# Kernel optimization log

Measured on AMD Instinct MI355X. Metric: run time of the kernel, lower is better.

The kernel has to match this reference:

```python
import jax, jax.numpy as jnp
import numpy as np

TOP_K = 2

def setup_inputs() -> dict:
    key = jax.random.key(0)
    k1, k2, k3, k4, k5 = jax.random.split(key, 5)
    B, S, D, E, H = 1, 2048, 2048, 8, 5632
    scale = 0.02
    return {
        "x": jax.random.normal(k1, (B, S, D), dtype=jnp.float32),
        "gate_w": jax.random.normal(k2, (E, D), dtype=jnp.float32) * scale,
        "w1": jax.random.normal(k3, (E, H, D), dtype=jnp.float32) * scale,
        "w2": jax.random.normal(k4, (E, D, H), dtype=jnp.float32) * scale,
        "w3": jax.random.normal(k5, (E, H, D), dtype=jnp.float32) * scale,
    }


def reference(x, gate_w, w1, w2, w3):
    # x: [B, S, D]; gate_w: [E, D]; w1/w3: [E, H, D]; w2: [E, D, H]
    B, S, D = x.shape
    E = gate_w.shape[0]
    xf = x.reshape(-1, D)                      # [T, D]
    T = xf.shape[0]

    # Gate (gate_softmax=False): topk on raw scores, softmax over the top-k
    scores = xf @ gate_w.T                     # [T, E]
    expert_weights, expert_indices = jax.lax.top_k(scores, TOP_K)
    expert_weights = jax.nn.softmax(expert_weights, axis=-1)  # [T, K]

    # Scatter top-k weights to a dense [T, E] combine matrix (zeros elsewhere)
    combine = jnp.zeros((T, E), dtype=xf.dtype).at[
        jnp.arange(T)[:, None], expert_indices
    ].add(expert_weights)

    # SwiGLU FFN per expert, batched over the (small, fixed) expert axis.
    # Math identical to masked dispatch since combine is zero off the top-k.
    h = jax.nn.silu(jnp.einsum("td,ehd->eth", xf, w1)) \
        * jnp.einsum("td,ehd->eth", xf, w3)    # [E, T, H]
    ye = jnp.einsum("eth,edh->etd", h, w2)     # [E, T, D]

    # Weighted combine of top-k expert outputs per token
    y = jnp.einsum("etd,te->td", ye, combine)  # [T, D]
    return y.reshape(B, S, D)
```

## Files before the change

kernel.cpp:

```cpp
#include <hip/hip_runtime.h>
#include <hip/hip_bf16.h>

#define T_TOK 2048
#define DIM   2048
#define NE    8
#define NH    5632

typedef __attribute__((ext_vector_type(4))) float f32x4;
typedef __attribute__((ext_vector_type(8))) short short8;
typedef __attribute__((ext_vector_type(4))) unsigned int u32x4;
typedef __attribute__((ext_vector_type(4))) float float4v;

__device__ inline unsigned short f2bf(float f) {
    unsigned u = __builtin_bit_cast(unsigned, f);
    u += 0x7fffu + ((u >> 16) & 1u);
    return (unsigned short)(u >> 16);
}

__device__ __forceinline__ short8 pack8(float4v a, float4v b) {
    short8 o;
    o[0]=(short)f2bf(a[0]); o[1]=(short)f2bf(a[1]); o[2]=(short)f2bf(a[2]); o[3]=(short)f2bf(a[3]);
    o[4]=(short)f2bf(b[0]); o[5]=(short)f2bf(b[1]); o[6]=(short)f2bf(b[2]); o[7]=(short)f2bf(b[3]);
    return o;
}

__device__ __forceinline__ short8 cvt8(f32x4 lo, f32x4 hi) {
    u32x4 L = __builtin_bit_cast(u32x4, lo);
    u32x4 H = __builtin_bit_cast(u32x4, hi);
    u32x4 r;
    r[0] = __builtin_amdgcn_perm(L[1], L[0], 0x07060302u);
    r[1] = __builtin_amdgcn_perm(L[3], L[2], 0x07060302u);
    r[2] = __builtin_amdgcn_perm(H[1], H[0], 0x07060302u);
    r[3] = __builtin_amdgcn_perm(H[3], H[2], 0x07060302u);
    return __builtin_bit_cast(short8, r);
}

__device__ __forceinline__ void glds16(const void* g, void* l) {
    __builtin_amdgcn_global_load_lds((const __attribute__((address_space(1))) void*)g,
                                     (__attribute__((address_space(3))) void*)l, 16, 0, 0);
}

__global__ void k_cvt(const float* __restrict__ src, unsigned short* __restrict__ dst, int n8) {
    int i = blockIdx.x * blockDim.x + threadIdx.x;
    if (i >= n8) return;
    const float4v* xv = (const float4v*)src;
    ((short8*)dst)[i] = pack8(xv[2 * i], xv[2 * i + 1]);
}

__global__ void k_gate(const float* __restrict__ x, const float* __restrict__ gw,
                       int* __restrict__ rt_e, float* __restrict__ rt_w, int* __restrict__ cnt) {
    int wid = threadIdx.x >> 6, lane = threadIdx.x & 63;
    int t = blockIdx.x * 4 + wid;
    if (t >= T_TOK) return;
    float acc[NE];
#pragma unroll
    for (int e = 0; e < NE; e++) acc[e] = 0.f;
    const float* xr = x + (size_t)t * DIM;
    for (int d = lane; d < DIM; d += 64) {
        float xv = xr[d];
#pragma unroll
        for (int e = 0; e < NE; e++) acc[e] += xv * gw[e * DIM + d];
    }
#pragma unroll
    for (int e = 0; e < NE; e++) {
        float v = acc[e];
#pragma unroll
        for (int off = 32; off; off >>= 1) v += __shfl_xor(v, off);
        acc[e] = v;
    }
    if (lane == 0) {
        int i0 = 0; float s0 = acc[0];
#pragma unroll
        for (int e = 1; e < NE; e++) if (acc[e] > s0) { s0 = acc[e]; i0 = e; }
        int i1 = -1; float s1 = -1e30f;
#pragma unroll
        for (int e = 0; e < NE; e++) if (e != i0 && acc[e] > s1) { s1 = acc[e]; i1 = e; }
        float w0 = 1.f / (1.f + expf(s1 - s0));
        rt_e[2 * t] = i0; rt_e[2 * t + 1] = i1;
        rt_w[2 * t] = w0; rt_w[2 * t + 1] = 1.f - w0;
        atomicAdd(&cnt[i0], 1);
        atomicAdd(&cnt[i1], 1);
    }
}

__global__ void k_base(const int* __restrict__ cnt, int* __restrict__ base, int* __restrict__ pb) {
    if (threadIdx.x == 0) {
        int s = 0, p = 0;
        for (int e = 0; e < NE; e++) {
            base[e] = s; pb[e] = p;
            s += cnt[e];
            p += ((cnt[e] + 127) >> 7) << 7;
        }
    }
}

__global__ void k_assign(const int* __restrict__ rt_e, const float* __restrict__ rt_w,
                         const int* __restrict__ base, int* __restrict__ run,
                         int* __restrict__ tok, float* __restrict__ tw) {
    int t = blockIdx.x * blockDim.x + threadIdx.x;
    if (t >= T_TOK) return;
#pragma unroll
    for (int k = 0; k < 2; k++) {
        int e = rt_e[2 * t + k];
        int p = atomicAdd(&run[e], 1);
        int g = base[e] + p;
        tok[g] = t;
        tw[g] = rt_w[2 * t + k];
    }
}

__global__ void k_xpack(const float* __restrict__ x,
                        const int* __restrict__ cnt, const int* __restrict__ base,
                        const int* __restrict__ pb, const int* __restrict__ tok,
                        unsigned short* __restrict__ xp) {
    int e = blockIdx.z, mt = blockIdx.y, kt = blockIdx.x;
    int c = cnt[e], m0 = mt * 128;
    if (m0 >= c) return;
    int gb = base[e];
    int ptile = (pb[e] >> 7) + mt;
    int lane = threadIdx.x & 63, w = threadIdx.x >> 6;
    int kc = lane & 7;
    unsigned short* db = xp + (size_t)ptile * 262144 + (size_t)kt * 8192;
#pragma unroll
    for (int it = 0; it < 4; ++it) {
        int rloc = it * 32 + w * 8 + (lane >> 3);
        int slot = m0 + rloc;
        int t = tok[gb + (slot < c ? slot : 0)];
        const float* s = x + (size_t)t * DIM + kt * 64 + kc * 8;
        *(short8*)(db + kc * 1024 + rloc * 8) = pack8(*(const float4v*)s, *(const float4v*)(s + 4));
    }
}

__launch_bounds__(256, 3)
__global__ void k_ffn1(const unsigned short* __restrict__ xp,
                       const float* __restrict__ w1, const float* __restrict__ w3,
                       const int* __restrict__ cnt, const int* __restrict__ pb,
                       unsigned short* __restrict__ hb, int nwg) {
    int bid = blockIdx.x;
    int swz = (bid & 7) * (nwg >> 3) + (bid >> 3);
    int mt = swz & 15;
    int r2 = swz >> 4;
    int nt = r2 % 88;
    int e  = r2 / 88;
    int c  = cnt[e];
    int m0 = mt * 128;
    if (m0 >= c) return;
    int ptile = (pb[e] >> 7) + mt;

    __shared__ unsigned short As[8192];
    __shared__ float B1f[4096];
    __shared__ float B3f[4096];

    int tid = threadIdx.x;
    int lane = tid & 63, w = tid >> 6;
    int wm = w >> 1, wn = w & 1;
    int half = w & 1, wh = w >> 1;
    int p15 = lane & 15, rl0 = lane >> 4;

    const unsigned short* aB = xp + (size_t)ptile * 262144 + half * 512 + lane * 8;
    const float* w1e = w1 + (size_t)(e * NH + nt * 64) * DIM;
    const float* w3e = w3 + (size_t)(e * NH + nt * 64) * DIM;

    f32x4 acc1[4][2], acc3[4][2];
#pragma unroll
    for (int i = 0; i < 4; i++)
#pragma unroll
        for (int j = 0; j < 2; j++) { acc1[i][j] = (f32x4)0.f; acc3[i][j] = (f32x4)0.f; }

    for (int kt = 0; kt < 32; ++kt) {
        __syncthreads();
#pragma unroll
        for (int i = 0; i < 4; i++) {
            int kc = i * 2 + wh;
            glds16(aB + kt * 8192 + kc * 1024, (char*)As + kc * 2048 + half * 1024);
        }
#pragma unroll
        for (int i = 0; i < 4; i++) {
            int rloc = w * 16 + i * 4 + rl0;
            int q    = p15 ^ ((i * 4 + rl0) & 15);
            glds16(w1e + (size_t)rloc * DIM + kt * 64 + q * 4, (char*)B1f + (w * 16 + i * 4) * 256);
            glds16(w3e + (size_t)rloc * DIM + kt * 64 + q * 4, (char*)B3f + (w * 16 + i * 4) * 256);
        }
        asm volatile("s_waitcnt vmcnt(0)" ::: "memory");
        __syncthreads();
#pragma unroll
        for (int kh = 0; kh < 2; kh++) {
            int kc = kh * 4 + rl0;
            short8 a[4], b1[2], b3[2];
#pragma unroll
            for (int mf = 0; mf < 4; mf++) {
                int r = wm * 64 + mf * 16 + p15;
                a[mf] = *(const short8*)(As + kc * 1024 + r * 8);
            }
#pragma unroll
            for (int nf = 0; nf < 2; nf++) {
                int rb = wn * 32 + nf * 16 + p15;
                const float* rB1 = B1f + rb * 64;
                const float* rB3 = B3f + rb * 64;
                int o0 = ((2 * kc) ^ p15) << 2, o1 = ((2 * kc + 1) ^ p15) << 2;
                b1[nf] = cvt8(*(const f32x4*)(rB1 + o0), *(const f32x4*)(rB1 + o1));
                b3[nf] = cvt8(*(const f32x4*)(rB3 + o0), *(const f32x4*)(rB3 + o1));
            }
#pragma unroll
            for (int mf = 0; mf < 4; mf++)
#pragma unroll
                for (int nf = 0; nf < 2; nf++) {
                    acc1[mf][nf] = __builtin_amdgcn_mfma_f32_16x16x32_bf16(a[mf], b1[nf], acc1[mf][nf], 0, 0, 0);
                    acc3[mf][nf] = __builtin_amdgcn_mfma_f32_16x16x32_bf16(a[mf], b3[nf], acc3[mf][nf], 0, 0, 0);
                }
        }
    }

    unsigned short* hT = hb + ((size_t)ptile * 88 + nt) * 8192;
#pragma unroll
    for (int mf = 0; mf < 4; mf++)
#pragma unroll
        for (int nf = 0; nf < 2; nf++)
#pragma unroll
            for (int r = 0; r < 4; r++) {
                int row = wm * 64 + mf * 16 + (rl0 << 2) + r;
                int col = wn * 32 + nf * 16 + p15;
                if (m0 + row < c) {
                    float a = acc1[mf][nf][r];
                    float g = a / (1.f + expf(-a));
                    float v = g * acc3[mf][nf][r];
                    hT[(col >> 3) * 1024 + row * 8 + (col & 7)] = f2bf(v);
                }
            }
}

__launch_bounds__(256, 3)
__global__ void k_ffn2(const unsigned short* __restrict__ hb,
                       const float* __restrict__ w2,
                       const int* __restrict__ cnt, const int* __restrict__ base,
                       const int* __restrict__ pb,
                       const int* __restrict__ tok, const float* __restrict__ tw,
                       float* __restrict__ y, int nwg) {
    int bid = blockIdx.x;
    int swz = (bid & 7) * (nwg >> 3) + (bid >> 3);
    int mt = swz & 15;
    int r2 = swz >> 4;
    int nt = r2 & 15;
    int e  = r2 >> 4;
    int c  = cnt[e];
    int m0 = mt * 128;
    if (m0 >= c) return;
    int gb = base[e];
    int ptile = (pb[e] >> 7) + mt;
    int n0 = nt * 128;

    __shared__ unsigned short As[8192];
    __shared__ float Bf[8192];
    __shared__ int   toks[128];
    __shared__ float gws[128];

    int tid = threadIdx.x;
    if (tid < 128) {
        int s = m0 + tid;
        toks[tid] = (s < c) ? tok[gb + s] : 0;
        gws[tid]  = (s < c) ? tw[gb + s] : 0.f;
    }

    int lane = tid & 63, w = tid >> 6;
    int wm = w >> 1, wn = w & 1;
    int half = w & 1, wh = w >> 1;
    int p15 = lane & 15, rl0 = lane >> 4;

    const unsigned short* aB = hb + (size_t)ptile * 720896 + half * 512 + lane * 8;
    const float* w2e = w2 + (size_t)(e * DIM + n0) * NH;

    f32x4 acc[4][4];
#pragma unroll
    for (int i = 0; i < 4; i++)
#pragma unroll
        for (int j = 0; j < 4; j++) acc[i][j] = (f32x4)0.f;

    for (int kt = 0; kt < 88; ++kt) {
        __syncthreads();
#pragma unroll
        for (int i = 0; i < 4; i++) {
            int kc = i * 2 + wh;
            glds16(aB + kt * 8192 + kc * 1024, (char*)As + kc * 2048 + half * 1024);
        }
#pragma unroll
        for (int i = 0; i < 8; i++) {
            int rloc = w * 32 + i * 4 + rl0;
            int q    = p15 ^ ((i * 4 + rl0) & 15);
            glds16(w2e + (size_t)rloc * NH + kt * 64 + q * 4, (char*)Bf + (w * 32 + i * 4) * 256);
        }
        asm volatile("s_waitcnt vmcnt(0)" ::: "memory");
        __syncthreads();
#pragma unroll
        for (int kh = 0; kh < 2; kh++) {
            int kc = kh * 4 + rl0;
            short8 a[4], b[4];
#pragma unroll
            for (int mf = 0; mf < 4; mf++) {
                int r = wm * 64 + mf * 16 + p15;
                a[mf] = *(const short8*)(As + kc * 1024 + r * 8);
            }
            int o0 = ((2 * kc) ^ p15) << 2, o1 = ((2 * kc + 1) ^ p15) << 2;
#pragma unroll
            for (int nf = 0; nf < 4; nf++) {
                int rb = wn * 64 + nf * 16 + p15;
                const float* rB = Bf + rb * 64;
                b[nf] = cvt8(*(const f32x4*)(rB + o0), *(const f32x4*)(rB + o1));
            }
#pragma unroll
            for (int mf = 0; mf < 4; mf++)
#pragma unroll
                for (int nf = 0; nf < 4; nf++)
                    acc[mf][nf] = __builtin_amdgcn_mfma_f32_16x16x32_bf16(a[mf], b[nf], acc[mf][nf], 0, 0, 0);
        }
    }

#pragma unroll
    for (int mf = 0; mf < 4; mf++)
#pragma unroll
        for (int nf = 0; nf < 4; nf++)
#pragma unroll
            for (int r = 0; r < 4; r++) {
                int row = wm * 64 + mf * 16 + (rl0 << 2) + r;
                int col = wn * 64 + nf * 16 + p15;
                if (m0 + row < c) {
                    float v = gws[row] * acc[mf][nf][r];
                    atomicAdd(&y[(size_t)toks[row] * DIM + n0 + col], v);
                }
            }
}

__launch_bounds__(256)
__global__ void k_ffn1_fb(const unsigned short* __restrict__ xb,
                          const float* __restrict__ w1, const float* __restrict__ w3,
                          const int* __restrict__ cnt, const int* __restrict__ base,
                          const int* __restrict__ tok, unsigned short* __restrict__ hbuf) {
    int e  = blockIdx.x >> 4;
    int mt = blockIdx.x & 15;
    int c  = cnt[e];
    int m0 = mt * 128;
    if (m0 >= c) return;
    int gb = base[e];
    int n0 = blockIdx.y * 64;

    __shared__ unsigned short As[128 * 64];
    __shared__ unsigned short B1s[64 * 64];
    __shared__ unsigned short B3s[64 * 64];
    __shared__ int toks[128];

    int tid = threadIdx.x;
    if (tid < 128) {
        int s = m0 + tid;
        toks[tid] = (s < c) ? tok[gb + s] : tok[gb];
    }
    int lane = tid & 63, wid = tid >> 6;
    int wm = wid >> 1, wn = wid & 1;

    f32x4 acc1[4][2], acc3[4][2];
#pragma unroll
    for (int i = 0; i < 4; i++)
#pragma unroll
        for (int j = 0; j < 2; j++) { acc1[i][j] = (f32x4)0.f; acc3[i][j] = (f32x4)0.f; }

    const float* W1 = w1 + (size_t)e * NH * DIM + (size_t)n0 * DIM;
    const float* W3 = w3 + (size_t)e * NH * DIM + (size_t)n0 * DIM;

    for (int kt = 0; kt < DIM / 64; ++kt) {
        int k0 = kt * 64;
        __syncthreads();
#pragma unroll
        for (int i = 0; i < 4; i++) {
            int f = i * 256 + tid;
            int row = f >> 3, ch = f & 7;
            u32x4 v = *(const u32x4*)(xb + (size_t)toks[row] * DIM + k0 + ch * 8);
            *(u32x4*)(As + row * 64 + ((ch ^ (row & 7)) << 3)) = v;
        }
#pragma unroll
        for (int i = 0; i < 2; i++) {
            int f = i * 256 + tid;
            int row = f >> 3, ch = f & 7;
            {
                const float* src = W1 + (size_t)row * DIM + k0 + ch * 8;
                *(short8*)(B1s + row * 64 + ((ch ^ (row & 7)) << 3)) =
                    pack8(*(const float4v*)src, *(const float4v*)(src + 4));
            }
            {
                const float* src = W3 + (size_t)row * DIM + k0 + ch * 8;
                *(short8*)(B3s + row * 64 + ((ch ^ (row & 7)) << 3)) =
                    pack8(*(const float4v*)src, *(const float4v*)(src + 4));
            }
        }
        __syncthreads();
#pragma unroll
        for (int kk = 0; kk < 2; kk++) {
            int kch = kk * 4 + (lane >> 4);
            short8 af[4], b1f[2], b3f[2];
#pragma unroll
            for (int mf = 0; mf < 4; mf++) {
                int r = wm * 64 + mf * 16 + (lane & 15);
                af[mf] = *(const short8*)(As + r * 64 + ((kch ^ (r & 7)) << 3));
            }
#pragma unroll
            for (int nf = 0; nf < 2; nf++) {
                int r = wn * 32 + nf * 16 + (lane & 15);
                b1f[nf] = *(const short8*)(B1s + r * 64 + ((kch ^ (r & 7)) << 3));
                b3f[nf] = *(const short8*)(B3s + r * 64 + ((kch ^ (r & 7)) << 3));
            }
#pragma unroll
            for (int mf = 0; mf < 4; mf++)
#pragma unroll
                for (int nf = 0; nf < 2; nf++) {
                    acc1[mf][nf] = __builtin_amdgcn_mfma_f32_16x16x32_bf16(af[mf], b1f[nf], acc1[mf][nf], 0, 0, 0);
                    acc3[mf][nf] = __builtin_amdgcn_mfma_f32_16x16x32_bf16(af[mf], b3f[nf], acc3[mf][nf], 0, 0, 0);
                }
        }
    }
#pragma unroll
    for (int mf = 0; mf < 4; mf++)
#pragma unroll
        for (int nf = 0; nf < 2; nf++)
#pragma unroll
            for (int r = 0; r < 4; r++) {
                int row = wm * 64 + mf * 16 + ((lane >> 4) << 2) + r;
                int col = wn * 32 + nf * 16 + (lane & 15);
                if (m0 + row < c) {
                    float a = acc1[mf][nf][r];
                    float g = a / (1.f + expf(-a));
                    float v = g * acc3[mf][nf][r];
                    hbuf[(size_t)(gb + m0 + row) * NH + n0 + col] = f2bf(v);
                }
            }
}

__launch_bounds__(256)
__global__ void k_ffn2_fb(const unsigned short* __restrict__ hbuf,
                          const float* __restrict__ w2,
                          const int* __restrict__ cnt, const int* __restrict__ base,
                          const int* __restrict__ tok, const float* __restrict__ tw,
                          float* __restrict__ y) {
    int e  = blockIdx.x >> 4;
    int mt = blockIdx.x & 15;
    int c  = cnt[e];
    int m0 = mt * 128;
    if (m0 >= c) return;
    int gb = base[e];
    int n0 = blockIdx.y * 128;

    __shared__ unsigned short As[128 * 64];
    __shared__ unsigned short Bs[128 * 64];
    __shared__ int   toks[128];
    __shared__ float gws[128];

    int tid = threadIdx.x;
    if (tid < 128) {
        int s = m0 + tid;
        toks[tid] = (s < c) ? tok[gb + s] : 0;
        gws[tid]  = (s < c) ? tw[gb + s] : 0.f;
    }
    int lane = tid & 63, wid = tid >> 6;
    int wm = wid >> 1, wn = wid & 1;

    f32x4 acc[4][4];
#pragma unroll
    for (int i = 0; i < 4; i++)
#pragma unroll
        for (int j = 0; j < 4; j++) acc[i][j] = (f32x4)0.f;

    const float* W2 = w2 + (size_t)e * DIM * NH + (size_t)n0 * NH;

    for (int kt = 0; kt < NH / 64; ++kt) {
        int k0 = kt * 64;
        __syncthreads();
#pragma unroll
        for (int i = 0; i < 4; i++) {
            int f = i * 256 + tid;
            int row = f >> 3, ch = f & 7;
            int rr = m0 + row; rr = (rr < c) ? rr : (c - 1);
            u32x4 v = *(const u32x4*)(hbuf + (size_t)(gb + rr) * NH + k0 + ch * 8);
            *(u32x4*)(As + row * 64 + ((ch ^ (row & 7)) << 3)) = v;
        }
#pragma unroll
        for (int i = 0; i < 4; i++) {
            int f = i * 256 + tid;
            int row = f >> 3, ch = f & 7;
            const float* src = W2 + (size_t)row * NH + k0 + ch * 8;
            *(short8*)(Bs + row * 64 + ((ch ^ (row & 7)) << 3)) =
                pack8(*(const float4v*)src, *(const float4v*)(src + 4));
        }
        __syncthreads();
#pragma unroll
        for (int kk = 0; kk < 2; kk++) {
            int kch = kk * 4 + (lane >> 4);
            short8 af[4], bf[4];
#pragma unroll
            for (int mf = 0; mf < 4; mf++) {
                int r = wm * 64 + mf * 16 + (lane & 15);
                af[mf] = *(const short8*)(As + r * 64 + ((kch ^ (r & 7)) << 3));
            }
#pragma unroll
            for (int nf = 0; nf < 4; nf++) {
                int r = wn * 64 + nf * 16 + (lane & 15);
                bf[nf] = *(const short8*)(Bs + r * 64 + ((kch ^ (r & 7)) << 3));
            }
#pragma unroll
            for (int mf = 0; mf < 4; mf++)
#pragma unroll
                for (int nf = 0; nf < 4; nf++)
                    acc[mf][nf] = __builtin_amdgcn_mfma_f32_16x16x32_bf16(af[mf], bf[nf], acc[mf][nf], 0, 0, 0);
        }
    }
#pragma unroll
    for (int mf = 0; mf < 4; mf++)
#pragma unroll
        for (int nf = 0; nf < 4; nf++)
#pragma unroll
            for (int r = 0; r < 4; r++) {
                int row = wm * 64 + mf * 16 + ((lane >> 4) << 2) + r;
                int col = wn * 64 + nf * 16 + (lane & 15);
                if (m0 + row < c) {
                    float v = gws[row] * acc[mf][nf][r];
                    atomicAdd(&y[(size_t)toks[row] * DIM + n0 + col], v);
                }
            }
}

extern "C" void kernel_launch(void* const* d_in, const int* in_sizes, int n_in,
                              void* d_out, int out_size, void* d_ws, size_t ws_size,
                              hipStream_t stream) {
    const float* x  = (const float*)d_in[0];
    const float* gw = (const float*)d_in[1];
    const float* w1 = (const float*)d_in[2];
    const float* w2 = (const float*)d_in[3];
    const float* w3 = (const float*)d_in[4];
    float* y = (float*)d_out;

    char* ws = (char*)d_ws;
    int*   cnt  = (int*)(ws + 0);
    int*   run  = (int*)(ws + 64);
    int*   basep= (int*)(ws + 128);
    int*   pb   = (int*)(ws + 192);
    int*   tok  = (int*)(ws + 256);
    float* tw   = (float*)(ws + 16640);
    int*   rt_e = (int*)(ws + 33024);
    float* rt_w = (float*)(ws + 49408);
    unsigned short* xp    = (unsigned short*)(ws + 66048);
    unsigned short* hbufp = (unsigned short*)(ws + 21037568);
    const size_t needed = 78709248ull;

    hipMemsetAsync(ws, 0, 256, stream);
    hipMemsetAsync(d_out, 0, (size_t)out_size * sizeof(float), stream);

    k_gate<<<T_TOK / 4, 256, 0, stream>>>(x, gw, rt_e, rt_w, cnt);
    k_base<<<1, 64, 0, stream>>>(cnt, basep, pb);
    k_assign<<<T_TOK / 256, 256, 0, stream>>>(rt_e, rt_w, basep, run, tok, tw);

    if (ws_size >= needed) {
        k_xpack<<<dim3(32, 16, NE), 256, 0, stream>>>(x, cnt, basep, pb, tok, xp);
        int nwg1 = NE * 16 * 88;
        int nwg2 = NE * 16 * 16;
        k_ffn1<<<nwg1, 256, 0, stream>>>(xp, w1, w3, cnt, pb, hbufp, nwg1);
        k_ffn2<<<nwg2, 256, 0, stream>>>(hbufp, w2, cnt, basep, pb, tok, tw, y, nwg2);
    } else {
        k_cvt<<<(T_TOK * DIM / 8) / 256, 256, 0, stream>>>(x, xp, T_TOK * DIM / 8);
        k_ffn1_fb<<<dim3(NE * 16, NH / 64), 256, 0, stream>>>(xp, w1, w3, cnt, basep, tok, hbufp);
        k_ffn2_fb<<<dim3(NE * 16, DIM / 128), 256, 0, stream>>>(hbufp, w2, cnt, basep, tok, tw, y);
    }
}
```

Baseline: 837.0 us.

## Pre-pack w2 into tiled bf16 layout before the second FFN GEMM

Adds a kernel that converts w2 from fp32 to bf16 in the same tiled layout the second GEMM consumes. k_ffn2 can then load its B tile with the same direct global-to-LDS copies used for A, removing the fp32 LDS buffer and the per-fragment conversion. With half the LDS footprint, the launch bound is raised to 4 workgroups per CU. The cost is a full extra pass that reads all of w2 and writes a bf16 copy on every call, plus a much larger workspace requirement. If the provided workspace is smaller than the new threshold, execution falls back to the slow path.

```diff
diff --git a/kernel.cpp b/kernel.cpp
--- a/kernel.cpp
+++ b/kernel.cpp
@@ -106,6 +106,20 @@
         int g = base[e] + p;
         tok[g] = t;
         tw[g] = rt_w[2 * t + k];
+    }
+}
+
+__global__ void k_packw2(const float* __restrict__ w2, unsigned short* __restrict__ w2p) {
+    int e = blockIdx.z, nt = blockIdx.y, kt = blockIdx.x;
+    int lane = threadIdx.x & 63, w = threadIdx.x >> 6;
+    int kc = lane & 7;
+    const float* sb = w2 + (size_t)e * DIM * NH;
+    unsigned short* db = w2p + ((size_t)(e * 16 + nt) * 88 + kt) * 8192;
+#pragma unroll
+    for (int it = 0; it < 4; ++it) {
+        int rloc = it * 32 + w * 8 + (lane >> 3);
+        const float* s = sb + (size_t)(nt * 128 + rloc) * NH + kt * 64 + kc * 8;
+        *(short8*)(db + kc * 1024 + rloc * 8) = pack8(*(const float4v*)s, *(const float4v*)(s + 4));
     }
 }
 
@@ -229,9 +243,9 @@
             }
 }
 
-__launch_bounds__(256, 3)
+__launch_bounds__(256, 4)
 __global__ void k_ffn2(const unsigned short* __restrict__ hb,
-                       const float* __restrict__ w2,
+                       const unsigned short* __restrict__ w2p,
                        const int* __restrict__ cnt, const int* __restrict__ base,
                        const int* __restrict__ pb,
                        const int* __restrict__ tok, const float* __restrict__ tw,
@@ -250,7 +264,7 @@
     int n0 = nt * 128;
 
     __shared__ unsigned short As[8192];
-    __shared__ float Bf[8192];
+    __shared__ unsigned short Bs[8192];
     __shared__ int   toks[128];
     __shared__ float gws[128];
 
@@ -264,10 +278,9 @@
     int lane = tid & 63, w = tid >> 6;
     int wm = w >> 1, wn = w & 1;
     int half = w & 1, wh = w >> 1;
-    int p15 = lane & 15, rl0 = lane >> 4;
-
-    const unsigned short* aB = hb + (size_t)ptile * 720896 + half * 512 + lane * 8;
-    const float* w2e = w2 + (size_t)(e * DIM + n0) * NH;
+
+    const unsigned short* aB = hb  + (size_t)ptile * 720896 + half * 512 + lane * 8;
+    const unsigned short* bB = w2p + (size_t)(e * 16 + nt) * 720896 + half * 512 + lane * 8;
 
     f32x4 acc[4][4];
 #pragma unroll
@@ -281,30 +294,23 @@
         for (int i = 0; i < 4; i++) {
             int kc = i * 2 + wh;
             glds16(aB + kt * 8192 + kc * 1024, (char*)As + kc * 2048 + half * 1024);
-        }
-#pragma unroll
-        for (int i = 0; i < 8; i++) {
-            int rloc = w * 32 + i * 4 + rl0;
-            int q    = p15 ^ ((i * 4 + rl0) & 15);
-            glds16(w2e + (size_t)rloc * NH + kt * 64 + q * 4, (char*)Bf + (w * 32 + i * 4) * 256);
+            glds16(bB + kt * 8192 + kc * 1024, (char*)Bs + kc * 2048 + half * 1024);
         }
         asm volatile("s_waitcnt vmcnt(0)" ::: "memory");
         __syncthreads();
 #pragma unroll
         for (int kh = 0; kh < 2; kh++) {
-            int kc = kh * 4 + rl0;
+            int kc = kh * 4 + (lane >> 4);
             short8 a[4], b[4];
 #pragma unroll
             for (int mf = 0; mf < 4; mf++) {
-                int r = wm * 64 + mf * 16 + p15;
+                int r = wm * 64 + mf * 16 + (lane & 15);
                 a[mf] = *(const short8*)(As + kc * 1024 + r * 8);
             }
-            int o0 = ((2 * kc) ^ p15) << 2, o1 = ((2 * kc + 1) ^ p15) << 2;
 #pragma unroll
             for (int nf = 0; nf < 4; nf++) {
-                int rb = wn * 64 + nf * 16 + p15;
-                const float* rB = Bf + rb * 64;
-                b[nf] = cvt8(*(const f32x4*)(rB + o0), *(const f32x4*)(rB + o1));
+                int rb = wn * 64 + nf * 16 + (lane & 15);
+                b[nf] = *(const short8*)(Bs + kc * 1024 + rb * 8);
             }
 #pragma unroll
             for (int mf = 0; mf < 4; mf++)
@@ -320,8 +326,8 @@
         for (int nf = 0; nf < 4; nf++)
 #pragma unroll
             for (int r = 0; r < 4; r++) {
-                int row = wm * 64 + mf * 16 + (rl0 << 2) + r;
-                int col = wn * 64 + nf * 16 + p15;
+                int row = wm * 64 + mf * 16 + ((lane >> 4) << 2) + r;
+                int col = wn * 64 + nf * 16 + (lane & 15);
                 if (m0 + row < c) {
                     float v = gws[row] * acc[mf][nf][r];
                     atomicAdd(&y[(size_t)toks[row] * DIM + n0 + col], v);
@@ -544,7 +550,8 @@
     float* rt_w = (float*)(ws + 49408);
     unsigned short* xp    = (unsigned short*)(ws + 66048);
     unsigned short* hbufp = (unsigned short*)(ws + 21037568);
-    const size_t needed = 78709248ull;
+    unsigned short* w2p   = (unsigned short*)(ws + 78709248);
+    const size_t needed = 263258624ull;
 
     hipMemsetAsync(ws, 0, 256, stream);
     hipMemsetAsync(d_out, 0, (size_t)out_size * sizeof(float), stream);
@@ -554,11 +561,12 @@
     k_assign<<<T_TOK / 256, 256, 0, stream>>>(rt_e, rt_w, basep, run, tok, tw);
 
     if (ws_size >= needed) {
+        k_packw2<<<dim3(88, 16, NE), 256, 0, stream>>>(w2, w2p);
         k_xpack<<<dim3(32, 16, NE), 256, 0, stream>>>(x, cnt, basep, pb, tok, xp);
         int nwg1 = NE * 16 * 88;
         int nwg2 = NE * 16 * 16;
         k_ffn1<<<nwg1, 256, 0, stream>>>(xp, w1, w3, cnt, pb, hbufp, nwg1);
-        k_ffn2<<<nwg2, 256, 0, stream>>>(hbufp, w2, cnt, basep, pb, tok, tw, y, nwg2);
+        k_ffn2<<<nwg2, 256, 0, stream>>>(hbufp, w2p, cnt, basep, pb, tok, tw, y, nwg2);
     } else {
         k_cvt<<<(T_TOK * DIM / 8) / 256, 256, 0, stream>>>(x, xp, T_TOK * DIM / 8);
         k_ffn1_fb<<<dim3(NE * 16, NH / 64), 256, 0, stream>>>(xp, w1, w3, cnt, basep, tok, hbufp);
```

After: 832.5 us. Within noise of the previous version (-0.5%).

## Convert fp32 weights to bf16 in registers before LDS store in both FFN kernels

Applied to the files above, without the earlier changes.

Weight tiles for the two FFN GEMMs are now loaded from global memory into registers, converted to bf16, and written to LDS in a new swizzled layout. Previously they were copied to LDS as fp32 through direct global-to-LDS loads and converted on every fragment read. This halves the LDS footprint, so the launch bounds rise from 3 to 4 blocks per CU, and the conversion is no longer repeated across waves. The cost is that weight loads now pass through registers and are waited on synchronously before the barrier, which adds register pressure and removes the async LDS-load path.

```diff
diff --git a/kernel.cpp b/kernel.cpp
--- a/kernel.cpp
+++ b/kernel.cpp
@@ -131,7 +131,7 @@
     }
 }
 
-__launch_bounds__(256, 3)
+__launch_bounds__(256, 4)
 __global__ void k_ffn1(const unsigned short* __restrict__ xp,
                        const float* __restrict__ w1, const float* __restrict__ w3,
                        const int* __restrict__ cnt, const int* __restrict__ pb,
@@ -148,8 +148,8 @@
     int ptile = (pb[e] >> 7) + mt;
 
     __shared__ unsigned short As[8192];
-    __shared__ float B1f[4096];
-    __shared__ float B3f[4096];
+    __shared__ unsigned short B1[4096];
+    __shared__ unsigned short B3[4096];
 
     int tid = threadIdx.x;
     int lane = tid & 63, w = tid >> 6;
@@ -158,8 +158,12 @@
     int p15 = lane & 15, rl0 = lane >> 4;
 
     const unsigned short* aB = xp + (size_t)ptile * 262144 + half * 512 + lane * 8;
-    const float* w1e = w1 + (size_t)(e * NH + nt * 64) * DIM;
-    const float* w3e = w3 + (size_t)(e * NH + nt * 64) * DIM;
+
+    int br = w * 16 + (lane >> 2);
+    int bp = lane & 3;
+    int srW = (br & 48) | ((br + 4 * bp) & 15);
+    const float* w1r = w1 + (size_t)(e * NH + nt * 64 + br) * DIM + bp * 16;
+    const float* w3r = w3 + (size_t)(e * NH + nt * 64 + br) * DIM + bp * 16;
 
     f32x4 acc1[4][2], acc3[4][2];
 #pragma unroll
@@ -174,18 +178,26 @@
             int kc = i * 2 + wh;
             glds16(aB + kt * 8192 + kc * 1024, (char*)As + kc * 2048 + half * 1024);
         }
-#pragma unroll
-        for (int i = 0; i < 4; i++) {
-            int rloc = w * 16 + i * 4 + rl0;
-            int q    = p15 ^ ((i * 4 + rl0) & 15);
-            glds16(w1e + (size_t)rloc * DIM + kt * 64 + q * 4, (char*)B1f + (w * 16 + i * 4) * 256);
-            glds16(w3e + (size_t)rloc * DIM + kt * 64 + q * 4, (char*)B3f + (w * 16 + i * 4) * 256);
+        {
+            const float* s = w1r + kt * 64;
+            f32x4 f0 = *(const f32x4*)s,       f1 = *(const f32x4*)(s + 4);
+            f32x4 f2 = *(const f32x4*)(s + 8), f3 = *(const f32x4*)(s + 12);
+            *(short8*)(B1 + (2 * bp) * 512 + srW * 8)     = cvt8(f0, f1);
+            *(short8*)(B1 + (2 * bp + 1) * 512 + srW * 8) = cvt8(f2, f3);
+        }
+        {
+            const float* s = w3r + kt * 64;
+            f32x4 f0 = *(const f32x4*)s,       f1 = *(const f32x4*)(s + 4);
+            f32x4 f2 = *(const f32x4*)(s + 8), f3 = *(const f32x4*)(s + 12);
+            *(short8*)(B3 + (2 * bp) * 512 + srW * 8)     = cvt8(f0, f1);
+            *(short8*)(B3 + (2 * bp + 1) * 512 + srW * 8) = cvt8(f2, f3);
         }
         asm volatile("s_waitcnt vmcnt(0)" ::: "memory");
         __syncthreads();
 #pragma unroll
         for (int kh = 0; kh < 2; kh++) {
             int kc = kh * 4 + rl0;
+            int sro = (p15 + 4 * (kc >> 1)) & 15;
             short8 a[4], b1[2], b3[2];
 #pragma unroll
             for (int mf = 0; mf < 4; mf++) {
@@ -194,12 +206,9 @@
             }
 #pragma unroll
             for (int nf = 0; nf < 2; nf++) {
-                int rb = wn * 32 + nf * 16 + p15;
-                const float* rB1 = B1f + rb * 64;
-                const float* rB3 = B3f + rb * 64;
-                int o0 = ((2 * kc) ^ p15) << 2, o1 = ((2 * kc + 1) ^ p15) << 2;
-                b1[nf] = cvt8(*(const f32x4*)(rB1 + o0), *(const f32x4*)(rB1 + o1));
-                b3[nf] = cvt8(*(const f32x4*)(rB3 + o0), *(const f32x4*)(rB3 + o1));
+                int rbase = wn * 32 + nf * 16;
+                b1[nf] = *(const short8*)(B1 + kc * 512 + (rbase + sro) * 8);
+                b3[nf] = *(const short8*)(B3 + kc * 512 + (rbase + sro) * 8);
             }
 #pragma unroll
             for (int mf = 0; mf < 4; mf++)
@@ -229,7 +238,7 @@
             }
 }
 
-__launch_bounds__(256, 3)
+__launch_bounds__(256, 4)
 __global__ void k_ffn2(const unsigned short* __restrict__ hb,
                        const float* __restrict__ w2,
                        const int* __restrict__ cnt, const int* __restrict__ base,
@@ -250,7 +259,7 @@
     int n0 = nt * 128;
 
     __shared__ unsigned short As[8192];
-    __shared__ float Bf[8192];
+    __shared__ unsigned short Bs[8192];
     __shared__ int   toks[128];
     __shared__ float gws[128];
 
@@ -267,7 +276,12 @@
     int p15 = lane & 15, rl0 = lane >> 4;
 
     const unsigned short* aB = hb + (size_t)ptile * 720896 + half * 512 + lane * 8;
-    const float* w2e = w2 + (size_t)(e * DIM + n0) * NH;
+
+    int br = tid >> 1;
+    int hh = tid & 1;
+    int sr0 = (br & 112) | ((br + 8 * hh) & 15);
+    int sr1 = (br & 112) | ((br + 8 * hh + 4) & 15);
+    const float* w2r = w2 + (size_t)(e * DIM + n0 + br) * NH + hh * 32;
 
     f32x4 acc[4][4];
 #pragma unroll
@@ -282,29 +296,33 @@
             int kc = i * 2 + wh;
             glds16(aB + kt * 8192 + kc * 1024, (char*)As + kc * 2048 + half * 1024);
         }
-#pragma unroll
-        for (int i = 0; i < 8; i++) {
-            int rloc = w * 32 + i * 4 + rl0;
-            int q    = p15 ^ ((i * 4 + rl0) & 15);
-            glds16(w2e + (size_t)rloc * NH + kt * 64 + q * 4, (char*)Bf + (w * 32 + i * 4) * 256);
+        {
+            const float* s = w2r + kt * 64;
+            f32x4 f0 = *(const f32x4*)s,       f1 = *(const f32x4*)(s + 4);
+            f32x4 f2 = *(const f32x4*)(s + 8), f3 = *(const f32x4*)(s + 12);
+            *(short8*)(Bs + (hh * 4 + 0) * 1024 + sr0 * 8) = cvt8(f0, f1);
+            *(short8*)(Bs + (hh * 4 + 1) * 1024 + sr0 * 8) = cvt8(f2, f3);
+            f0 = *(const f32x4*)(s + 16); f1 = *(const f32x4*)(s + 20);
+            f2 = *(const f32x4*)(s + 24); f3 = *(const f32x4*)(s + 28);
+            *(short8*)(Bs + (hh * 4 + 2) * 1024 + sr1 * 8) = cvt8(f0, f1);
+            *(short8*)(Bs + (hh * 4 + 3) * 1024 + sr1 * 8) = cvt8(f2, f3);
         }
         asm volatile("s_waitcnt vmcnt(0)" ::: "memory");
         __syncthreads();
 #pragma unroll
         for (int kh = 0; kh < 2; kh++) {
             int kc = kh * 4 + rl0;
+            int sro = (p15 + 4 * (kc >> 1)) & 15;
             short8 a[4], b[4];
 #pragma unroll
             for (int mf = 0; mf < 4; mf++) {
                 int r = wm * 64 + mf * 16 + p15;
                 a[mf] = *(const short8*)(As + kc * 1024 + r * 8);
             }
-            int o0 = ((2 * kc) ^ p15) << 2, o1 = ((2 * kc + 1) ^ p15) << 2;
 #pragma unroll
             for (int nf = 0; nf < 4; nf++) {
-                int rb = wn * 64 + nf * 16 + p15;
-                const float* rB = Bf + rb * 64;
-                b[nf] = cvt8(*(const f32x4*)(rB + o0), *(const f32x4*)(rB + o1));
+                int rbase = wn * 64 + nf * 16;
+                b[nf] = *(const short8*)(Bs + kc * 1024 + (rbase + sro) * 8);
             }
 #pragma unroll
             for (int mf = 0; mf < 4; mf++)
```

Measured after the change: 1.153 ms. 1.38x slower.
